# Performance work log

Hardware: AMD Instinct MI355X
Metric: run time of the kernel (lower is better)

Reference implementation:

```python
import jax, jax.numpy as jnp
import numpy as np

DIM = 1024
HEADS = 16
HEAD_DIM = DIM // HEADS
SCALE = HEAD_DIM ** -0.5


def setup_inputs() -> dict:
    key = jax.random.key(0)
    k_x, k_wqkv, k_bqkv, k_wp, k_bp = jax.random.split(key, 5)
    B, N, C = 8, 1024, DIM
    lim_qkv = 1.0 / np.sqrt(C)
    x = jax.random.normal(k_x, (B, N, C), dtype=jnp.float32)
    # store weights in [in, out] layout (torch Linear weight is [out,in]; y = x @ W.T + b)
    W_qkv = jax.random.uniform(k_wqkv, (C, 3 * C), dtype=jnp.float32, minval=-lim_qkv, maxval=lim_qkv)
    b_qkv = jax.random.uniform(k_bqkv, (3 * C,), dtype=jnp.float32, minval=-lim_qkv, maxval=lim_qkv)
    W_proj = jax.random.uniform(k_wp, (C, C), dtype=jnp.float32, minval=-lim_qkv, maxval=lim_qkv)
    b_proj = jax.random.uniform(k_bp, (C,), dtype=jnp.float32, minval=-lim_qkv, maxval=lim_qkv)
    return {"x": x, "W_qkv": W_qkv, "b_qkv": b_qkv, "W_proj": W_proj, "b_proj": b_proj}


def reference(x, W_qkv, b_qkv, W_proj, b_proj):
    B, N, C = x.shape
    H, D = HEADS, C // HEADS
    qkv = x @ W_qkv + b_qkv                          # [B, N, 3C]
    qkv = qkv.reshape(B, N, 3, H, D)
    q, k, v = jnp.moveaxis(qkv, 2, 0)                # each [B, N, H, D]
    q = q.transpose(0, 2, 1, 3)                      # [B, H, N, D]
    k = k.transpose(0, 2, 1, 3)
    v = v.transpose(0, 2, 1, 3)
    attn = jnp.einsum("bhnd,bhmd->bhnm", q, k) * SCALE
    attn = jax.nn.softmax(attn, axis=-1)
    out = jnp.einsum("bhnm,bhmd->bhnd", attn, v)     # [B, H, N, D]
    out = out.transpose(0, 2, 1, 3).reshape(B, N, C)
    return out @ W_proj + b_proj
```

## Files before the change

kernel.cpp:

```cpp
#include <hip/hip_runtime.h>
#include <hip/hip_bf16.h>


using bf16x8 = __attribute__((ext_vector_type(8))) short;
using f32x4  = __attribute__((ext_vector_type(4))) float;
using u16    = unsigned short;
using u16x4  = __attribute__((ext_vector_type(4))) unsigned short;
using u16x8  = __attribute__((ext_vector_type(8))) unsigned short;

__device__ __forceinline__ u16 f2bf(float f) {
  unsigned int u = __float_as_uint(f);
  u += 0x7FFFu + ((u >> 16) & 1u);
  return (u16)(u >> 16);
}
__device__ __forceinline__ float bf2f(u16 h) {
  return __uint_as_float(((unsigned int)h) << 16);
}

__device__ __forceinline__ void gload16(const u16* g, u16* lbase, int lane) {
#if __has_builtin(__builtin_amdgcn_global_load_lds)
  __builtin_amdgcn_global_load_lds(
      (const __attribute__((address_space(1))) void*)g,
      (__attribute__((address_space(3))) void*)lbase, 16, 0, 0);
#else
  *(u16x8*)(lbase + (size_t)lane * 8) = *(const u16x8*)g;
#endif
}

__global__ __launch_bounds__(256) void convert_f32_bf16(
    const float* __restrict__ in, u16* __restrict__ out)
{
  size_t i = ((size_t)blockIdx.x * 256 + threadIdx.x) * 8;
  f32x4 a = *(const f32x4*)(in + i);
  f32x4 b = *(const f32x4*)(in + i + 4);
  u16x8 h = { f2bf(a.x), f2bf(a.y), f2bf(a.z), f2bf(a.w),
              f2bf(b.x), f2bf(b.y), f2bf(b.z), f2bf(b.w) };
  *(u16x8*)(out + i) = h;
}

__global__ __launch_bounds__(256) void transpose_w(
    const float* __restrict__ W, u16* __restrict__ Wt, int K, int N)
{
  __shared__ float T[64][65];
  const int t = threadIdx.x;
  const int n0 = blockIdx.x * 64, k0 = blockIdx.y * 64;
  const int r = t >> 4, c4 = (t & 15) * 4;
  #pragma unroll
  for (int i = 0; i < 4; ++i) {
    f32x4 v = *(const f32x4*)&W[(size_t)(k0 + r + i * 16) * N + n0 + c4];
    T[r + i * 16][c4 + 0] = v.x;
    T[r + i * 16][c4 + 1] = v.y;
    T[r + i * 16][c4 + 2] = v.z;
    T[r + i * 16][c4 + 3] = v.w;
  }
  __syncthreads();
  const int nr = t >> 2, cs = (t & 3) * 16;
  u16x8 h0, h1;
  #pragma unroll
  for (int j = 0; j < 8; ++j) h0[j] = f2bf(T[cs + j][nr]);
  #pragma unroll
  for (int j = 0; j < 8; ++j) h1[j] = f2bf(T[cs + 8 + j][nr]);
  u16* dst = Wt + (size_t)(n0 + nr) * K + k0 + cs;
  *(u16x8*)dst = h0;
  *(u16x8*)(dst + 8) = h1;
}

__global__ __launch_bounds__(256, 2) void qkv_gemm2(
    const u16* __restrict__ Xb, const u16* __restrict__ Wt,
    const float* __restrict__ bias,
    u16* __restrict__ Qb, u16* __restrict__ Kb, u16* __restrict__ VtG)
{
  constexpr int KD = 1024;
  __shared__ __align__(16) u16 As[128 * 32];
  __shared__ __align__(16) u16 Bs[128 * 32];

  const int tid = threadIdx.x;
  const int lane = tid & 63, wid = tid >> 6;
  const int wr = wid >> 1, wc = wid & 1;
  const int lg = lane >> 4, lc = lane & 15;
  const int row0 = blockIdx.x * 128, col0 = blockIdx.y * 128;

  f32x4 acc[4][4];
  #pragma unroll
  for (int m = 0; m < 4; ++m)
    #pragma unroll
    for (int n = 0; n < 4; ++n) acc[m][n] = (f32x4){0.f, 0.f, 0.f, 0.f};

  const int l4 = lane >> 2, ls = (lane & 3) * 8;
  const u16* gA0 = Xb + (size_t)(row0 + wid * 16 + l4) * KD + ls;
  const u16* gB0 = Wt + (size_t)(col0 + wid * 16 + l4) * KD + ls;
  u16* lA0 = As + wid * 512;
  u16* lB0 = Bs + wid * 512;

  for (int k0 = 0; k0 < KD; k0 += 32) {
    gload16(gA0 + k0, lA0, lane);
    gload16(gA0 + 64 * KD + k0, lA0 + 2048, lane);
    gload16(gB0 + k0, lB0, lane);
    gload16(gB0 + 64 * KD + k0, lB0 + 2048, lane);
    __syncthreads();

    bf16x8 a[4], b[4];
    #pragma unroll
    for (int m = 0; m < 4; ++m)
      a[m] = *(const bf16x8*)(As + (wr * 64 + m * 16 + lc) * 32 + lg * 8);
    #pragma unroll
    for (int n = 0; n < 4; ++n)
      b[n] = *(const bf16x8*)(Bs + (wc * 64 + n * 16 + lc) * 32 + lg * 8);
    #pragma unroll
    for (int m = 0; m < 4; ++m)
      #pragma unroll
      for (int n = 0; n < 4; ++n)
        acc[m][n] = __builtin_amdgcn_mfma_f32_16x16x32_bf16(a[m], b[n], acc[m][n], 0, 0, 0);
    __syncthreads();
  }

  #pragma unroll
  for (int m = 0; m < 4; ++m) {
    #pragma unroll
    for (int n = 0; n < 4; ++n) {
      const int gcb = col0 + wc * 64 + n * 16;
      const int which = gcb >> 10;
      const int gc = gcb + lc;
      const float bv = bias[gc];
      const int ci = gc & 1023, h = ci >> 6, d = ci & 63;
      const int gr0 = row0 + wr * 64 + m * 16 + lg * 4;
      const int bb = gr0 >> 10, nn0 = gr0 & 1023;
      if (which == 2) {
        u16x4 pv = { f2bf(acc[m][n][0] + bv), f2bf(acc[m][n][1] + bv),
                     f2bf(acc[m][n][2] + bv), f2bf(acc[m][n][3] + bv) };
        *(u16x4*)&VtG[((size_t)(bb * 16 + h) * 64 + d) * 1024 + nn0] = pv;
      } else {
        u16* dst = (which == 0) ? Qb : Kb;
        #pragma unroll
        for (int r = 0; r < 4; ++r)
          dst[((size_t)(bb * 16 + h) * 1024 + nn0 + r) * 64 + d] =
              f2bf(acc[m][n][r] + bv);
      }
    }
  }
}

__global__ __launch_bounds__(256, 2) void attn_kernel(
    const u16* __restrict__ Q, const u16* __restrict__ K,
    const u16* __restrict__ Vt, u16* __restrict__ O)
{
  __shared__ __align__(16) u16 Ks[64 * 64];
  __shared__ __align__(16) u16 Vs[64 * 64];
  __shared__ __align__(16) u16 Pl[4 * 32 * 72];

  const int tid = threadIdx.x, lane = tid & 63, wid = tid >> 6;
  const int lg = lane >> 4, lc = lane & 15;
  const int bh = blockIdx.x;
  const int qt = blockIdx.y;
  const size_t base = (size_t)bh * 65536;
  const u16* Qp = Q + base;
  const u16* Kp = K + base;
  const u16* Vp = Vt + base;

  bf16x8 qf[2][2];
  #pragma unroll
  for (int f = 0; f < 2; ++f) {
    const u16* qsrc = Qp + (size_t)(qt * 128 + wid * 32 + f * 16 + lc) * 64 + lg * 8;
    #pragma unroll
    for (int ks = 0; ks < 2; ++ks) {
      u16x8 raw = *(const u16x8*)(qsrc + ks * 32);
      bf16x8 t;
      #pragma unroll
      for (int j = 0; j < 8; ++j) t[j] = (short)f2bf(bf2f(raw[j]) * 0.125f);
      qf[f][ks] = t;
    }
  }

  f32x4 o[2][4];
  #pragma unroll
  for (int f = 0; f < 2; ++f)
    #pragma unroll
    for (int d = 0; d < 4; ++d) o[f][d] = (f32x4){0.f, 0.f, 0.f, 0.f};
  float m_r[2] = {-1e30f, -1e30f};
  float l_r[2] = {0.f, 0.f};

  const int srow  = lane >> 3;
  const int sslot = (lane & 7) ^ srow;
  const u16* gK0 = Kp + (size_t)(wid * 16 + srow) * 64 + sslot * 8;
  const u16* gV0 = Vp + (size_t)(wid * 16 + srow) * 1024 + sslot * 8;
  u16* lK0 = Ks + wid * 1024;
  u16* lV0 = Vs + wid * 1024;

  const int xr = lc & 7;
  const int cof0 = ((0 + lg) ^ xr) * 8;
  const int cof1 = ((4 + lg) ^ xr) * 8;
  const int prow = (wid * 32 + lc) * 72;

  for (int kt = 0; kt < 16; ++kt) {
    gload16(gK0 + kt * 4096, lK0, lane);
    gload16(gK0 + kt * 4096 + 512, lK0 + 512, lane);
    gload16(gV0 + kt * 64, lV0, lane);
    gload16(gV0 + 8192 + kt * 64, lV0 + 512, lane);
    __syncthreads();

    f32x4 s[2][4];
    #pragma unroll
    for (int f = 0; f < 2; ++f)
      #pragma unroll
      for (int kb = 0; kb < 4; ++kb) s[f][kb] = (f32x4){0.f, 0.f, 0.f, 0.f};
    #pragma unroll
    for (int ks = 0; ks < 2; ++ks) {
      const int co = ks ? cof1 : cof0;
      #pragma unroll
      for (int kb = 0; kb < 4; ++kb) {
        bf16x8 kfr = *(const bf16x8*)(Ks + (kb * 16 + lc) * 64 + co);
        s[0][kb] = __builtin_amdgcn_mfma_f32_16x16x32_bf16(kfr, qf[0][ks], s[0][kb], 0, 0, 0);
        s[1][kb] = __builtin_amdgcn_mfma_f32_16x16x32_bf16(kfr, qf[1][ks], s[1][kb], 0, 0, 0);
      }
    }

    #pragma unroll
    for (int f = 0; f < 2; ++f) {
      f32x4 t01, t23;
      #pragma unroll
      for (int c = 0; c < 4; ++c) {
        t01[c] = fmaxf(s[f][0][c], s[f][1][c]);
        t23[c] = fmaxf(s[f][2][c], s[f][3][c]);
      }
      float t = fmaxf(fmaxf(fmaxf(t01[0], t01[1]), fmaxf(t01[2], t01[3])),
                      fmaxf(fmaxf(t23[0], t23[1]), fmaxf(t23[2], t23[3])));
      t = fmaxf(t, __shfl_xor(t, 16));
      t = fmaxf(t, __shfl_xor(t, 32));

      if (!__all((t - m_r[f]) <= 8.0f)) {
        float nm = fmaxf(m_r[f], t);
        float sc = __expf(m_r[f] - nm);
        m_r[f] = nm;
        l_r[f] *= sc;
        #pragma unroll
        for (int r = 0; r < 4; ++r) {
          float scr = __shfl(sc, lg * 4 + r, 16);
          #pragma unroll
          for (int d = 0; d < 4; ++d) o[f][d][r] *= scr;
        }
      }

      float lsum = 0.f;
      #pragma unroll
      for (int kb = 0; kb < 4; ++kb) {
        f32x4 p;
        #pragma unroll
        for (int c = 0; c < 4; ++c) {
          p[c] = __expf(s[f][kb][c] - m_r[f]);
          lsum += p[c];
        }
        unsigned w0 = (unsigned)f2bf(p[0]) | ((unsigned)f2bf(p[1]) << 16);
        unsigned w1 = (unsigned)f2bf(p[2]) | ((unsigned)f2bf(p[3]) << 16);
        int pe = prow + f * 16 * 72 + kb * 16 + lg * 4;
        *(unsigned*)(Pl + pe)     = w0;
        *(unsigned*)(Pl + pe + 2) = w1;
      }
      lsum += __shfl_xor(lsum, 16);
      lsum += __shfl_xor(lsum, 32);
      l_r[f] += lsum;
    }

    asm volatile("s_waitcnt lgkmcnt(0)" ::: "memory");
    __builtin_amdgcn_sched_barrier(0);

    bf16x8 pa[2][2];
    #pragma unroll
    for (int f = 0; f < 2; ++f)
      #pragma unroll
      for (int ks = 0; ks < 2; ++ks)
        pa[f][ks] = *(const bf16x8*)(Pl + prow + f * 16 * 72 + ks * 32 + lg * 8);
    #pragma unroll
    for (int d = 0; d < 4; ++d) {
      #pragma unroll
      for (int ks = 0; ks < 2; ++ks) {
        const int co = ks ? cof1 : cof0;
        bf16x8 vfr = *(const bf16x8*)(Vs + (d * 16 + lc) * 64 + co);
        o[0][d] = __builtin_amdgcn_mfma_f32_16x16x32_bf16(pa[0][ks], vfr, o[0][d], 0, 0, 0);
        o[1][d] = __builtin_amdgcn_mfma_f32_16x16x32_bf16(pa[1][ks], vfr, o[1][d], 0, 0, 0);
      }
    }
    __syncthreads();
  }

  const int b = bh >> 4, h = bh & 15;
  #pragma unroll
  for (int f = 0; f < 2; ++f) {
    float linv = 1.0f / l_r[f];
    #pragma unroll
    for (int r = 0; r < 4; ++r) {
      float li = __shfl(linv, lg * 4 + r, 16);
      int n = qt * 128 + wid * 32 + f * 16 + lg * 4 + r;
      u16* dst = O + ((size_t)b * 1024 + n) * 1024 + h * 64 + lc;
      #pragma unroll
      for (int d = 0; d < 4; ++d) dst[d * 16] = f2bf(o[f][d][r] * li);
    }
  }
}

__global__ __launch_bounds__(256, 2) void proj_gemm2(
    const u16* __restrict__ Ab, const u16* __restrict__ Wt,
    const float* __restrict__ bias, float* __restrict__ Out)
{
  constexpr int KD = 1024, NCOL = 1024;
  __shared__ __align__(16) u16 As[128 * 32];
  __shared__ __align__(16) u16 Bs[128 * 32];

  const int tid = threadIdx.x;
  const int lane = tid & 63, wid = tid >> 6;
  const int wr = wid >> 1, wc = wid & 1;
  const int lg = lane >> 4, lc = lane & 15;
  const int row0 = blockIdx.x * 128, col0 = blockIdx.y * 128;

  f32x4 acc[4][4];
  #pragma unroll
  for (int m = 0; m < 4; ++m)
    #pragma unroll
    for (int n = 0; n < 4; ++n) acc[m][n] = (f32x4){0.f, 0.f, 0.f, 0.f};

  const int l4 = lane >> 2, ls = (lane & 3) * 8;
  const u16* gA0 = Ab + (size_t)(row0 + wid * 16 + l4) * KD + ls;
  const u16* gB0 = Wt + (size_t)(col0 + wid * 16 + l4) * KD + ls;
  u16* lA0 = As + wid * 512;
  u16* lB0 = Bs + wid * 512;

  for (int k0 = 0; k0 < KD; k0 += 32) {
    gload16(gA0 + k0, lA0, lane);
    gload16(gA0 + 64 * KD + k0, lA0 + 2048, lane);
    gload16(gB0 + k0, lB0, lane);
    gload16(gB0 + 64 * KD + k0, lB0 + 2048, lane);
    __syncthreads();

    bf16x8 a[4], b[4];
    #pragma unroll
    for (int m = 0; m < 4; ++m)
      a[m] = *(const bf16x8*)(As + (wr * 64 + m * 16 + lc) * 32 + lg * 8);
    #pragma unroll
    for (int n = 0; n < 4; ++n)
      b[n] = *(const bf16x8*)(Bs + (wc * 64 + n * 16 + lc) * 32 + lg * 8);
    #pragma unroll
    for (int m = 0; m < 4; ++m)
      #pragma unroll
      for (int n = 0; n < 4; ++n)
        acc[m][n] = __builtin_amdgcn_mfma_f32_16x16x32_bf16(a[m], b[n], acc[m][n], 0, 0, 0);
    __syncthreads();
  }

  #pragma unroll
  for (int m = 0; m < 4; ++m) {
    #pragma unroll
    for (int n = 0; n < 4; ++n) {
      #pragma unroll
      for (int r = 0; r < 4; ++r) {
        int gr = row0 + wr * 64 + m * 16 + lg * 4 + r;
        int gc = col0 + wc * 64 + n * 16 + lc;
        Out[(size_t)gr * NCOL + gc] = acc[m][n][r] + bias[gc];
      }
    }
  }
}

extern "C" void kernel_launch(void* const* d_in, const int* in_sizes, int n_in,
                              void* d_out, int out_size, void* d_ws, size_t ws_size,
                              hipStream_t stream) {
  const float* x     = (const float*)d_in[0];
  const float* W_qkv = (const float*)d_in[1];
  const float* b_qkv = (const float*)d_in[2];
  const float* W_prj = (const float*)d_in[3];
  const float* b_prj = (const float*)d_in[4];
  float* out = (float*)d_out;

  const size_t SEG = (size_t)8192 * 1024;
  char* ws = (char*)d_ws;
  u16* Xb  = (u16*)ws;
  u16* Ab  = Xb;
  u16* VtG = (u16*)(ws + SEG * 2);
  u16* Wqt = (u16*)(ws + SEG * 4);
  u16* Wpt = Wqt + (size_t)3072 * 1024;
  u16* Qb  = (u16*)d_out;
  u16* Kb  = Qb + SEG;

  convert_f32_bf16<<<4096, 256, 0, stream>>>(x, Xb);
  transpose_w<<<dim3(48, 16), 256, 0, stream>>>(W_qkv, Wqt, 1024, 3072);
  transpose_w<<<dim3(16, 16), 256, 0, stream>>>(W_prj, Wpt, 1024, 1024);
  qkv_gemm2<<<dim3(64, 24), 256, 0, stream>>>(Xb, Wqt, b_qkv, Qb, Kb, VtG);
  attn_kernel<<<dim3(128, 8), 256, 0, stream>>>(Qb, Kb, VtG, Ab);
  proj_gemm2<<<dim3(64, 8), 256, 0, stream>>>(Ab, Wpt, b_prj, out);
}
```

Before: 171.3 us.

## Double-buffer K/V tiles in attention and move V transpose into separate kernel

The attention kernel now double-buffers its K and V tiles in LDS, prefetching the next tile with async global-to-LDS loads while the current tile is computed, and uses explicit vmcnt waits with raw barriers. The QKV GEMM epilogue now writes V in row layout like Q and K. A new v_transpose kernel then builds the transposed V layout, replacing the scattered transposed stores in the GEMM epilogue. This adds an extra launch and an extra pass over V in memory, and doubles the LDS used for K/V, which may affect occupancy.

```diff
diff --git a/kernel.cpp b/kernel.cpp
--- a/kernel.cpp
+++ b/kernel.cpp
@@ -65,10 +65,32 @@
   *(u16x8*)(dst + 8) = h1;
 }
 
+__global__ __launch_bounds__(256) void v_transpose(
+    const u16* __restrict__ Vr, u16* __restrict__ Vt)
+{
+  __shared__ u16 T[64 * 70];
+  const int bh = blockIdx.x >> 4, nc = blockIdx.x & 15;
+  const int t = threadIdx.x;
+  const int r = t >> 2, c = (t & 3) * 16;
+  const u16* src = Vr + ((size_t)bh * 1024 + nc * 64 + r) * 64 + c;
+  *(u16x8*)&T[r * 70 + c]     = *(const u16x8*)src;
+  *(u16x8*)&T[r * 70 + c + 8] = *(const u16x8*)(src + 8);
+  __syncthreads();
+  const int d = t >> 2, n0 = (t & 3) * 16;
+  u16x8 o0, o1;
+  #pragma unroll
+  for (int j = 0; j < 8; ++j) o0[j] = T[(n0 + j) * 70 + d];
+  #pragma unroll
+  for (int j = 0; j < 8; ++j) o1[j] = T[(n0 + 8 + j) * 70 + d];
+  u16* dst = Vt + ((size_t)bh * 64 + d) * 1024 + nc * 64 + n0;
+  *(u16x8*)dst = o0;
+  *(u16x8*)(dst + 8) = o1;
+}
+
 __global__ __launch_bounds__(256, 2) void qkv_gemm2(
     const u16* __restrict__ Xb, const u16* __restrict__ Wt,
     const float* __restrict__ bias,
-    u16* __restrict__ Qb, u16* __restrict__ Kb, u16* __restrict__ VtG)
+    u16* __restrict__ Qb, u16* __restrict__ Kb, u16* __restrict__ Vr)
 {
   constexpr int KD = 1024;
   __shared__ __align__(16) u16 As[128 * 32];
@@ -125,17 +147,11 @@
       const int ci = gc & 1023, h = ci >> 6, d = ci & 63;
       const int gr0 = row0 + wr * 64 + m * 16 + lg * 4;
       const int bb = gr0 >> 10, nn0 = gr0 & 1023;
-      if (which == 2) {
-        u16x4 pv = { f2bf(acc[m][n][0] + bv), f2bf(acc[m][n][1] + bv),
-                     f2bf(acc[m][n][2] + bv), f2bf(acc[m][n][3] + bv) };
-        *(u16x4*)&VtG[((size_t)(bb * 16 + h) * 64 + d) * 1024 + nn0] = pv;
-      } else {
-        u16* dst = (which == 0) ? Qb : Kb;
-        #pragma unroll
-        for (int r = 0; r < 4; ++r)
-          dst[((size_t)(bb * 16 + h) * 1024 + nn0 + r) * 64 + d] =
-              f2bf(acc[m][n][r] + bv);
-      }
+      u16* dst = (which == 0) ? Qb : (which == 1) ? Kb : Vr;
+      #pragma unroll
+      for (int r = 0; r < 4; ++r)
+        dst[((size_t)(bb * 16 + h) * 1024 + nn0 + r) * 64 + d] =
+            f2bf(acc[m][n][r] + bv);
     }
   }
 }
@@ -144,8 +160,8 @@
     const u16* __restrict__ Q, const u16* __restrict__ K,
     const u16* __restrict__ Vt, u16* __restrict__ O)
 {
-  __shared__ __align__(16) u16 Ks[64 * 64];
-  __shared__ __align__(16) u16 Vs[64 * 64];
+  __shared__ __align__(16) u16 Ks[2 * 64 * 64];
+  __shared__ __align__(16) u16 Vs[2 * 64 * 64];
   __shared__ __align__(16) u16 Pl[4 * 32 * 72];
 
   const int tid = threadIdx.x, lane = tid & 63, wid = tid >> 6;
@@ -157,28 +173,6 @@
   const u16* Kp = K + base;
   const u16* Vp = Vt + base;
 
-  bf16x8 qf[2][2];
-  #pragma unroll
-  for (int f = 0; f < 2; ++f) {
-    const u16* qsrc = Qp + (size_t)(qt * 128 + wid * 32 + f * 16 + lc) * 64 + lg * 8;
-    #pragma unroll
-    for (int ks = 0; ks < 2; ++ks) {
-      u16x8 raw = *(const u16x8*)(qsrc + ks * 32);
-      bf16x8 t;
-      #pragma unroll
-      for (int j = 0; j < 8; ++j) t[j] = (short)f2bf(bf2f(raw[j]) * 0.125f);
-      qf[f][ks] = t;
-    }
-  }
-
-  f32x4 o[2][4];
-  #pragma unroll
-  for (int f = 0; f < 2; ++f)
-    #pragma unroll
-    for (int d = 0; d < 4; ++d) o[f][d] = (f32x4){0.f, 0.f, 0.f, 0.f};
-  float m_r[2] = {-1e30f, -1e30f};
-  float l_r[2] = {0.f, 0.f};
-
   const int srow  = lane >> 3;
   const int sslot = (lane & 7) ^ srow;
   const u16* gK0 = Kp + (size_t)(wid * 16 + srow) * 64 + sslot * 8;
@@ -186,17 +180,52 @@
   u16* lK0 = Ks + wid * 1024;
   u16* lV0 = Vs + wid * 1024;
 
+  gload16(gK0, lK0, lane);
+  gload16(gK0 + 512, lK0 + 512, lane);
+  gload16(gV0, lV0, lane);
+  gload16(gV0 + 8192, lV0 + 512, lane);
+
+  bf16x8 qf[2][2];
+  #pragma unroll
+  for (int f = 0; f < 2; ++f) {
+    const u16* qsrc = Qp + (size_t)(qt * 128 + wid * 32 + f * 16 + lc) * 64 + lg * 8;
+    #pragma unroll
+    for (int ks = 0; ks < 2; ++ks) {
+      u16x8 raw = *(const u16x8*)(qsrc + ks * 32);
+      bf16x8 t;
+      #pragma unroll
+      for (int j = 0; j < 8; ++j) t[j] = (short)f2bf(bf2f(raw[j]) * 0.125f);
+      qf[f][ks] = t;
+    }
+  }
+
+  f32x4 o[2][4];
+  #pragma unroll
+  for (int f = 0; f < 2; ++f)
+    #pragma unroll
+    for (int d = 0; d < 4; ++d) o[f][d] = (f32x4){0.f, 0.f, 0.f, 0.f};
+  float m_r[2] = {-1e30f, -1e30f};
+  float l_r[2] = {0.f, 0.f};
+
   const int xr = lc & 7;
   const int cof0 = ((0 + lg) ^ xr) * 8;
   const int cof1 = ((4 + lg) ^ xr) * 8;
   const int prow = (wid * 32 + lc) * 72;
 
   for (int kt = 0; kt < 16; ++kt) {
-    gload16(gK0 + kt * 4096, lK0, lane);
-    gload16(gK0 + kt * 4096 + 512, lK0 + 512, lane);
-    gload16(gV0 + kt * 64, lV0, lane);
-    gload16(gV0 + 8192 + kt * 64, lV0 + 512, lane);
-    __syncthreads();
+    const int cOff = (kt & 1) * 4096;
+    const int nOff = cOff ^ 4096;
+    if (kt < 15) {
+      gload16(gK0 + (kt + 1) * 4096,       lK0 + nOff,       lane);
+      gload16(gK0 + (kt + 1) * 4096 + 512, lK0 + nOff + 512, lane);
+      gload16(gV0 + (kt + 1) * 64,         lV0 + nOff,       lane);
+      gload16(gV0 + (kt + 1) * 64 + 8192,  lV0 + nOff + 512, lane);
+      asm volatile("s_waitcnt vmcnt(4)" ::: "memory");
+    } else {
+      asm volatile("s_waitcnt vmcnt(0)" ::: "memory");
+    }
+    __builtin_amdgcn_s_barrier();
+    __builtin_amdgcn_sched_barrier(0);
 
     f32x4 s[2][4];
     #pragma unroll
@@ -208,7 +237,7 @@
       const int co = ks ? cof1 : cof0;
       #pragma unroll
       for (int kb = 0; kb < 4; ++kb) {
-        bf16x8 kfr = *(const bf16x8*)(Ks + (kb * 16 + lc) * 64 + co);
+        bf16x8 kfr = *(const bf16x8*)(Ks + cOff + (kb * 16 + lc) * 64 + co);
         s[0][kb] = __builtin_amdgcn_mfma_f32_16x16x32_bf16(kfr, qf[0][ks], s[0][kb], 0, 0, 0);
         s[1][kb] = __builtin_amdgcn_mfma_f32_16x16x32_bf16(kfr, qf[1][ks], s[1][kb], 0, 0, 0);
       }
@@ -274,12 +303,13 @@
       #pragma unroll
       for (int ks = 0; ks < 2; ++ks) {
         const int co = ks ? cof1 : cof0;
-        bf16x8 vfr = *(const bf16x8*)(Vs + (d * 16 + lc) * 64 + co);
+        bf16x8 vfr = *(const bf16x8*)(Vs + cOff + (d * 16 + lc) * 64 + co);
         o[0][d] = __builtin_amdgcn_mfma_f32_16x16x32_bf16(pa[0][ks], vfr, o[0][d], 0, 0, 0);
         o[1][d] = __builtin_amdgcn_mfma_f32_16x16x32_bf16(pa[1][ks], vfr, o[1][d], 0, 0, 0);
       }
     }
-    __syncthreads();
+    __builtin_amdgcn_s_barrier();
+    __builtin_amdgcn_sched_barrier(0);
   }
 
   const int b = bh >> 4, h = bh & 15;
@@ -376,13 +406,15 @@
   u16* VtG = (u16*)(ws + SEG * 2);
   u16* Wqt = (u16*)(ws + SEG * 4);
   u16* Wpt = Wqt + (size_t)3072 * 1024;
+  u16* Vr  = (u16*)(ws + 41943040);
   u16* Qb  = (u16*)d_out;
   u16* Kb  = Qb + SEG;
 
   convert_f32_bf16<<<4096, 256, 0, stream>>>(x, Xb);
   transpose_w<<<dim3(48, 16), 256, 0, stream>>>(W_qkv, Wqt, 1024, 3072);
   transpose_w<<<dim3(16, 16), 256, 0, stream>>>(W_prj, Wpt, 1024, 1024);
-  qkv_gemm2<<<dim3(64, 24), 256, 0, stream>>>(Xb, Wqt, b_qkv, Qb, Kb, VtG);
+  qkv_gemm2<<<dim3(64, 24), 256, 0, stream>>>(Xb, Wqt, b_qkv, Qb, Kb, Vr);
+  v_transpose<<<2048, 256, 0, stream>>>(Vr, VtG);
   attn_kernel<<<dim3(128, 8), 256, 0, stream>>>(Qb, Kb, VtG, Ab);
   proj_gemm2<<<dim3(64, 8), 256, 0, stream>>>(Ab, Wpt, b_prj, out);
 }
```

After: 181.9 us. 1.06x slower.
